# Kernel tuning notes

Hardware: AMD Instinct MI355X
Metric: run time of the kernel (lower is better)

Reference implementation:

```python
import jax, jax.numpy as jnp
import numpy as np
import math

EPS = 1e-5

def _ln(x):
    # LayerNorm over last dim, no affine (elementwise_affine=False)
    m = jnp.mean(x, axis=-1, keepdims=True)
    v = jnp.var(x, axis=-1, keepdims=True)
    return (x - m) / jnp.sqrt(v + EPS)

def setup_inputs() -> dict:
    key = jax.random.key(0)
    ks = jax.random.split(key, 12)
    bs, P, L, D, H, V = 32, 256, 32, 128, 128, 300
    std = 1.0 / math.sqrt(H)
    xav = math.sqrt(2.0 / ((V + 1) + D))
    emb = jax.random.normal(ks[2], (V + 1, D), jnp.float32) * xav
    emb = emb.at[V].set(0.0)  # padding_idx row
    u = lambda k, shp: jax.random.uniform(k, shp, jnp.float32, -std, std)
    return {
        "paths": jax.random.randint(ks[0], (bs, P, L), 0, V + 1),
        "paths_mask": jax.random.randint(ks[1], (bs, P), 1, L + 1),
        "emb": emb,
        "Wi": u(ks[3], (2 * H, D)), "bi": u(ks[4], (2 * H,)),
        "Wh": u(ks[5], (2 * H, H)), "bh": u(ks[6], (2 * H,)),
        "Ww": u(ks[7], (H, D)), "bw": u(ks[8], (H,)),
        "Wu": u(ks[9], (H, H)), "bu": u(ks[10], (H,)),
        "gamma": jnp.ones((2 * H,), jnp.float32),
        "beta": jnp.zeros((2 * H,), jnp.float32),
    }

def reference(paths, paths_mask, emb, Wi, bi, Wh, bh, Ww, bw, Wu, bu, gamma, beta):
    bs, P, L = paths.shape
    D = emb.shape[1]
    H = Ww.shape[0]
    B = bs * P
    # Embed and flatten paths: [L, B, D] (time-major for scan)
    x = emb[paths].reshape(B * L and (B, L, D))  # [B, L, D]
    x = jnp.transpose(x, (1, 0, 2))              # [L, B, D]
    # Input-dependent parts precomputed across all timesteps
    xi = _ln(jnp.einsum('lbd,gd->lbg', x, Wi) + bi)  # [L, B, 2H]
    xw = _ln(jnp.einsum('lbd,hd->lbh', x, Ww) + bw)  # [L, B, H]

    def step(h, xs_t):
        i2h_t, xw_t = xs_t
        h2h = _ln(h @ Wh.T + bh)
        gates = jax.nn.sigmoid(i2h_t + h2h)
        z = gates[:, :H]
        r = gates[:, H:]
        hu = _ln(h @ Wu.T + bu)
        h_hat = jnp.tanh(xw_t + r * hu)
        h_new = (1.0 - z) * h + z * h_hat
        return h_new, h_new

    h0 = jnp.zeros((B, H), x.dtype)
    _, ys = jax.lax.scan(step, h0, (xi, xw))      # ys: [L, B, H]
    lengths = paths_mask.reshape(-1)              # [B]
    out = ys[lengths - 1, jnp.arange(B)]          # [B, H] hidden at last valid step
    out = out.reshape(bs, P, H)
    # interleave forward/backward halves (relation-path pairing)
    fwd = jnp.concatenate([out[:, 0::2, :], out[:, 1::2, :]], axis=-1)
    bwd = jnp.concatenate([out[:, 1::2, :], out[:, 0::2, :]], axis=-1)
    res = jnp.zeros((bs, P, 2 * H), out.dtype)
    res = res.at[:, 0::2, :].set(fwd).at[:, 1::2, :].set(bwd)
    # final affine LayerNorm (gru_ln)
    m = jnp.mean(res, axis=-1, keepdims=True)
    v = jnp.var(res, axis=-1, keepdims=True)
    return (res - m) / jnp.sqrt(v + EPS) * gamma + beta
```

## Files before the change

### kernel.cpp

```cpp
#include <hip/hip_runtime.h>

typedef float  f32x4 __attribute__((ext_vector_type(4)));
typedef short  s16x8 __attribute__((ext_vector_type(8)));

__device__ __forceinline__ unsigned short bfb(float x) {
  unsigned u = __builtin_bit_cast(unsigned, x);
  return (unsigned short)((u + 0x7FFFu + ((u >> 16) & 1u)) >> 16);
}
__device__ __forceinline__ float fast_sig(float x) {
  float e = __builtin_amdgcn_exp2f(x * -1.44269504f);
  return __builtin_amdgcn_rcpf(1.f + e);
}
__device__ __forceinline__ float fast_tanh(float x) {
  float e = __builtin_amdgcn_exp2f(x * 2.88539008f);
  return 1.f - 2.f * __builtin_amdgcn_rcpf(1.f + e);
}

__global__ __launch_bounds__(1024) void sort_kernel(
    const int* __restrict__ pmask, int* __restrict__ perm)
{
  __shared__ int hist[33];
  __shared__ int base[33];
  const int tid = threadIdx.x;
  if (tid < 33) hist[tid] = 0;
  __syncthreads();
  for (int i = tid; i < 8192; i += 1024) atomicAdd(&hist[pmask[i]], 1);
  __syncthreads();
  if (tid == 0) {
    int acc = 0;
    for (int l = 1; l <= 32; ++l) { base[l] = acc; acc += hist[l]; }
  }
  __syncthreads();
  for (int i = tid; i < 8192; i += 1024) {
    const int pos = atomicAdd(&base[pmask[i]], 1);
    perm[pos] = i;
  }
}

__global__ __launch_bounds__(256) void tab_kernel(
    const float* __restrict__ emb,
    const float* __restrict__ Wi, const float* __restrict__ bi,
    const float* __restrict__ Ww, const float* __restrict__ bw,
    const float* __restrict__ Wh, const float* __restrict__ Wu,
    float* __restrict__ xi_tab, float* __restrict__ xw_tab,
    s16x8* __restrict__ frags)
{
  if (blockIdx.x >= 301) {
    const int T = blockIdx.x - 301;
    const int lane = threadIdx.x;
    if (lane >= 64) return;
    const int a = lane & 15, s = lane >> 4;
    const float* rowp[3];
    rowp[0] = Wh + (16 * T + a) * 128;
    rowp[1] = Wh + (128 + 16 * T + a) * 128;
    rowp[2] = Wu + (16 * T + a) * 128;
    #pragma unroll
    for (int mat = 0; mat < 3; ++mat) {
      #pragma unroll
      for (int kk = 0; kk < 4; ++kk) {
        const float* src = rowp[mat] + 32 * kk + 8 * s;
        const float4 A = *(const float4*)src;
        const float4 B = *(const float4*)(src + 4);
        s16x8 v;
        v[0] = (short)bfb(A.x); v[1] = (short)bfb(A.y);
        v[2] = (short)bfb(A.z); v[3] = (short)bfb(A.w);
        v[4] = (short)bfb(B.x); v[5] = (short)bfb(B.y);
        v[6] = (short)bfb(B.z); v[7] = (short)bfb(B.w);
        frags[((mat * 8 + T) * 4 + kk) * 64 + lane] = v;
      }
    }
    return;
  }

  const int v = blockIdx.x;
  const int g = threadIdx.x;
  const float4* er = (const float4*)(emb + v * 128);

  float acc = bi[g];
  const float4* wr = (const float4*)(Wi + g * 128);
  #pragma unroll 8
  for (int j = 0; j < 32; ++j) {
    float4 e = er[j], w4 = wr[j];
    acc = fmaf(e.x, w4.x, acc); acc = fmaf(e.y, w4.y, acc);
    acc = fmaf(e.z, w4.z, acc); acc = fmaf(e.w, w4.w, acc);
  }
  float accw = 0.f;
  if (g < 128) {
    accw = bw[g];
    const float4* wr2 = (const float4*)(Ww + g * 128);
    #pragma unroll 8
    for (int j = 0; j < 32; ++j) {
      float4 e = er[j], w4 = wr2[j];
      accw = fmaf(e.x, w4.x, accw); accw = fmaf(e.y, w4.y, accw);
      accw = fmaf(e.z, w4.z, accw); accw = fmaf(e.w, w4.w, accw);
    }
  }
  __shared__ float rs[4][2], rw[2][2];
  float s = acc, q = acc * acc;
  #pragma unroll
  for (int m = 1; m < 64; m <<= 1) { s += __shfl_xor(s, m); q += __shfl_xor(q, m); }
  if ((threadIdx.x & 63) == 0) { rs[threadIdx.x >> 6][0] = s; rs[threadIdx.x >> 6][1] = q; }
  float sw_ = accw, qw_ = accw * accw;
  #pragma unroll
  for (int m = 1; m < 64; m <<= 1) { sw_ += __shfl_xor(sw_, m); qw_ += __shfl_xor(qw_, m); }
  if (g < 128 && (g & 63) == 0) { rw[g >> 6][0] = sw_; rw[g >> 6][1] = qw_; }
  __syncthreads();
  const float SH = rs[0][0] + rs[1][0] + rs[2][0] + rs[3][0];
  const float QH = rs[0][1] + rs[1][1] + rs[2][1] + rs[3][1];
  const float mH = SH * (1.f / 256.f);
  const float rH = rsqrtf(fmaxf(QH * (1.f / 256.f) - mH * mH, 0.f) + 1e-5f);
  xi_tab[v * 256 + g] = (acc - mH) * rH;
  if (g < 128) {
    const float SW = rw[0][0] + rw[1][0], QW = rw[0][1] + rw[1][1];
    const float mW = SW * (1.f / 128.f);
    const float rW = rsqrtf(fmaxf(QW * (1.f / 128.f) - mW * mW, 0.f) + 1e-5f);
    xw_tab[v * 128 + g] = (accw - mW) * rW;
  }
}

__global__ __launch_bounds__(256, 2) void rec_kernel(
    const int* __restrict__ paths, const int* __restrict__ pmask,
    const int* __restrict__ perm,
    const float* __restrict__ bh, const float* __restrict__ bu,
    const float* __restrict__ xi_tab, const float* __restrict__ xw_tab,
    const s16x8* __restrict__ frags,
    float* __restrict__ out)
{
  __shared__ unsigned char hbuf[4096];
  __shared__ alignas(16) float red[4][16][4];
  __shared__ int plT[512];

  const int tid  = threadIdx.x;
  const int w    = tid >> 6;
  const int lane = tid & 63;
  const int s    = lane >> 4;
  const int r    = lane & 15;
  const int grp  = (blockIdx.x < 256) ? blockIdx.x : 767 - blockIdx.x;
  const int base = grp * 16;
  const int gb0  = 32 * w + 4 * s;

  s16x8 wz[2][4], wr2[2][4], wu2[2][4];
  #pragma unroll
  for (int u = 0; u < 2; ++u) {
    const int T = 2 * w + u;
    #pragma unroll
    for (int kk = 0; kk < 4; ++kk) {
      wz[u][kk]  = frags[((0 * 8 + T) * 4 + kk) * 64 + lane];
      wr2[u][kk] = frags[((1 * 8 + T) * 4 + kk) * 64 + lane];
      wu2[u][kk] = frags[((2 * 8 + T) * 4 + kk) * 64 + lane];
    }
  }

  for (int k = tid; k < 512; k += 256)
    plT[(k >> 4) * 16 + (k & 15)] = paths[perm[base + (k & 15)] * 32 + (k >> 4)];
  ((uint4*)hbuf)[tid] = uint4{0u, 0u, 0u, 0u};

  const int ri  = perm[base + r];
  const int len = pmask[ri];
  const int len_max = __shfl(len, 15);

  f32x4 bz[2], br2[2], bu2[2];
  #pragma unroll
  for (int u = 0; u < 2; ++u) {
    bz[u]  = *(const f32x4*)(bh + gb0 + 16 * u);
    br2[u] = *(const f32x4*)(bh + 128 + gb0 + 16 * u);
    bu2[u] = *(const f32x4*)(bu + gb0 + 16 * u);
  }

  int hoff[4];
  #pragma unroll
  for (int kk = 0; kk < 4; ++kk)
    hoff[kk] = r * 256 + (((4 * kk + s) ^ r) << 4);
  int hwadr[2];
  #pragma unroll
  for (int u = 0; u < 2; ++u)
    hwadr[u] = r * 256 + (((4 * w + 2 * u + (s >> 1)) ^ r) << 4) + (s & 1) * 8;

  float hreg[2][4] = {{0.f, 0.f, 0.f, 0.f}, {0.f, 0.f, 0.f, 0.f}};
  float* orow = out + (size_t)ri * 256 + gb0;

  __syncthreads();

  f32x4 xiz[2], xir[2], xwv[2];
  {
    const int p = plT[r];
    #pragma unroll
    for (int u = 0; u < 2; ++u) {
      xiz[u] = *(const f32x4*)(xi_tab + p * 256 + gb0 + 16 * u);
      xir[u] = *(const f32x4*)(xi_tab + p * 256 + 128 + gb0 + 16 * u);
      xwv[u] = *(const f32x4*)(xw_tab + p * 128 + gb0 + 16 * u);
    }
  }

  #pragma unroll 1
  for (int t = 0; t < len_max; ++t) {
    f32x4 az[2] = {}, ar[2] = {}, au[2] = {};
    #pragma unroll
    for (int kk = 0; kk < 4; ++kk) {
      const s16x8 hb = *(const s16x8*)(hbuf + hoff[kk]);
      #pragma unroll
      for (int u = 0; u < 2; ++u) {
        az[u] = __builtin_amdgcn_mfma_f32_16x16x32_bf16(wz[u][kk],  hb, az[u], 0, 0, 0);
        ar[u] = __builtin_amdgcn_mfma_f32_16x16x32_bf16(wr2[u][kk], hb, ar[u], 0, 0, 0);
        au[u] = __builtin_amdgcn_mfma_f32_16x16x32_bf16(wu2[u][kk], hb, au[u], 0, 0, 0);
      }
    }

    float sH = 0.f, qH = 0.f, sU = 0.f, qU = 0.f;
    #pragma unroll
    for (int u = 0; u < 2; ++u) {
      #pragma unroll
      for (int i = 0; i < 4; ++i) {
        az[u][i] += bz[u][i];  sH += az[u][i]; qH = fmaf(az[u][i], az[u][i], qH);
        ar[u][i] += br2[u][i]; sH += ar[u][i]; qH = fmaf(ar[u][i], ar[u][i], qH);
        au[u][i] += bu2[u][i]; sU += au[u][i]; qU = fmaf(au[u][i], au[u][i], qU);
      }
    }
    sH += __shfl_xor(sH, 16); qH += __shfl_xor(qH, 16);
    sU += __shfl_xor(sU, 16); qU += __shfl_xor(qU, 16);
    sH += __shfl_xor(sH, 32); qH += __shfl_xor(qH, 32);
    sU += __shfl_xor(sU, 32); qU += __shfl_xor(qU, 32);
    if (lane < 16) *(f32x4*)&red[w][r][0] = f32x4{sH, qH, sU, qU};

    const int tn = (t + 1 < len_max) ? t + 1 : t;
    const int pn = plT[tn * 16 + r];
    f32x4 nxiz[2], nxir[2], nxwv[2];
    #pragma unroll
    for (int u = 0; u < 2; ++u) {
      nxiz[u] = *(const f32x4*)(xi_tab + pn * 256 + gb0 + 16 * u);
      nxir[u] = *(const f32x4*)(xi_tab + pn * 256 + 128 + gb0 + 16 * u);
      nxwv[u] = *(const f32x4*)(xw_tab + pn * 128 + gb0 + 16 * u);
    }

    __syncthreads();

    float SH = 0.f, QH = 0.f, SU = 0.f, QU = 0.f;
    #pragma unroll
    for (int ww = 0; ww < 4; ++ww) {
      const f32x4 rr4 = *(const f32x4*)&red[ww][r][0];
      SH += rr4[0]; QH += rr4[1]; SU += rr4[2]; QU += rr4[3];
    }
    const float mH = SH * (1.f / 256.f);
    const float rsH = rsqrtf(fmaxf(QH * (1.f / 256.f) - mH * mH, 0.f) + 1e-5f);
    const float cH = -mH * rsH;
    const float mU = SU * (1.f / 128.f);
    const float rsU = rsqrtf(fmaxf(QU * (1.f / 128.f) - mU * mU, 0.f) + 1e-5f);
    const float cU = -mU * rsU;

    float hn[2][4];
    #pragma unroll
    for (int u = 0; u < 2; ++u) {
      #pragma unroll
      for (int i = 0; i < 4; ++i) {
        const float zg = fast_sig(xiz[u][i] + fmaf(az[u][i], rsH, cH));
        const float rg = fast_sig(xir[u][i] + fmaf(ar[u][i], rsH, cH));
        const float hu = fmaf(au[u][i], rsU, cU);
        const float hh = fast_tanh(fmaf(rg, hu, xwv[u][i]));
        hn[u][i] = fmaf(zg, hh - hreg[u][i], hreg[u][i]);
      }
    }
    if (t == len - 1) {
      #pragma unroll
      for (int u = 0; u < 2; ++u)
        *(float4*)(orow + 16 * u) = float4{hn[u][0], hn[u][1], hn[u][2], hn[u][3]};
    }

    #pragma unroll
    for (int u = 0; u < 2; ++u) {
      const unsigned lo  = (unsigned)bfb(hn[u][0]) | ((unsigned)bfb(hn[u][1]) << 16);
      const unsigned hi2 = (unsigned)bfb(hn[u][2]) | ((unsigned)bfb(hn[u][3]) << 16);
      *(uint2*)(hbuf + hwadr[u]) = uint2{lo, hi2};
      #pragma unroll
      for (int i = 0; i < 4; ++i) hreg[u][i] = hn[u][i];
      xiz[u] = nxiz[u]; xir[u] = nxir[u]; xwv[u] = nxwv[u];
    }
    __syncthreads();
  }
}

__global__ __launch_bounds__(256) void out_kernel(
    const float* __restrict__ gamma, const float* __restrict__ beta,
    float* __restrict__ out)
{
  const int tid = threadIdx.x;
  const int lane = tid & 63;
  const int m = blockIdx.x * 4 + (tid >> 6);
  float* pa = out + (size_t)(2 * m) * 256;
  float* pb = pa + 256;
  const float oa0 = pa[lane], oa1 = pa[64 + lane];
  const float ob0 = pb[lane], ob1 = pb[64 + lane];
  float s = oa0 + oa1 + ob0 + ob1;
  float q = oa0 * oa0 + oa1 * oa1 + ob0 * ob0 + ob1 * ob1;
  #pragma unroll
  for (int msk = 1; msk < 64; msk <<= 1) { s += __shfl_xor(s, msk); q += __shfl_xor(q, msk); }
  const float mean = s * (1.f / 256.f);
  const float rstd = rsqrtf(fmaxf(q * (1.f / 256.f) - mean * mean, 0.f) + 1e-5f);
  const float g0 = gamma[lane], g1 = gamma[64 + lane], g2 = gamma[128 + lane], g3 = gamma[192 + lane];
  const float b0 = beta[lane],  b1 = beta[64 + lane],  b2 = beta[128 + lane],  b3 = beta[192 + lane];
  const float na0 = (oa0 - mean) * rstd, na1 = (oa1 - mean) * rstd;
  const float nb0 = (ob0 - mean) * rstd, nb1 = (ob1 - mean) * rstd;
  pa[lane]       = na0 * g0 + b0;
  pa[64 + lane]  = na1 * g1 + b1;
  pa[128 + lane] = nb0 * g2 + b2;
  pa[192 + lane] = nb1 * g3 + b3;
  pb[lane]       = nb0 * g0 + b0;
  pb[64 + lane]  = nb1 * g1 + b1;
  pb[128 + lane] = na0 * g2 + b2;
  pb[192 + lane] = na1 * g3 + b3;
}

extern "C" void kernel_launch(void* const* d_in, const int* in_sizes, int n_in,
                              void* d_out, int out_size, void* d_ws, size_t ws_size,
                              hipStream_t stream) {
  const int*   paths = (const int*)d_in[0];
  const int*   pmask = (const int*)d_in[1];
  const float* emb   = (const float*)d_in[2];
  const float* Wi    = (const float*)d_in[3];
  const float* bi    = (const float*)d_in[4];
  const float* Wh    = (const float*)d_in[5];
  const float* bh    = (const float*)d_in[6];
  const float* Ww    = (const float*)d_in[7];
  const float* bw    = (const float*)d_in[8];
  const float* Wu    = (const float*)d_in[9];
  const float* bu    = (const float*)d_in[10];
  const float* gamma = (const float*)d_in[11];
  const float* beta  = (const float*)d_in[12];
  float* out = (float*)d_out;

  float* xi_tab = (float*)d_ws;
  float* xw_tab = xi_tab + 301 * 256;
  s16x8* frags  = (s16x8*)((char*)d_ws + 462336);
  int*   perm   = (int*)((char*)d_ws + 560640);

  hipLaunchKernelGGL(sort_kernel, dim3(1), dim3(1024), 0, stream, pmask, perm);
  hipLaunchKernelGGL(tab_kernel, dim3(309), dim3(256), 0, stream,
                     emb, Wi, bi, Ww, bw, Wh, Wu, xi_tab, xw_tab, frags);
  hipLaunchKernelGGL(rec_kernel, dim3(512), dim3(256), 0, stream,
                     paths, pmask, perm, bh, bu, xi_tab, xw_tab, frags, out);
  hipLaunchKernelGGL(out_kernel, dim3(1024), dim3(256), 0, stream, gamma, beta, out);
}
```

Before: 76.70 us.

## Fold sort into table kernel, replace shuffle reduction with LDS partials, hoist prefetch

After: 75.17 us. -2.0%, faster.

```diff
diff --git a/kernel.cpp b/kernel.cpp
--- a/kernel.cpp
+++ b/kernel.cpp
@@ -14,27 +14,6 @@
 __device__ __forceinline__ float fast_tanh(float x) {
   float e = __builtin_amdgcn_exp2f(x * 2.88539008f);
   return 1.f - 2.f * __builtin_amdgcn_rcpf(1.f + e);
-}
-
-__global__ __launch_bounds__(1024) void sort_kernel(
-    const int* __restrict__ pmask, int* __restrict__ perm)
-{
-  __shared__ int hist[33];
-  __shared__ int base[33];
-  const int tid = threadIdx.x;
-  if (tid < 33) hist[tid] = 0;
-  __syncthreads();
-  for (int i = tid; i < 8192; i += 1024) atomicAdd(&hist[pmask[i]], 1);
-  __syncthreads();
-  if (tid == 0) {
-    int acc = 0;
-    for (int l = 1; l <= 32; ++l) { base[l] = acc; acc += hist[l]; }
-  }
-  __syncthreads();
-  for (int i = tid; i < 8192; i += 1024) {
-    const int pos = atomicAdd(&base[pmask[i]], 1);
-    perm[pos] = i;
-  }
 }
 
 __global__ __launch_bounds__(256) void tab_kernel(
@@ -42,9 +21,29 @@
     const float* __restrict__ Wi, const float* __restrict__ bi,
     const float* __restrict__ Ww, const float* __restrict__ bw,
     const float* __restrict__ Wh, const float* __restrict__ Wu,
+    const int* __restrict__ pmask, int* __restrict__ perm,
     float* __restrict__ xi_tab, float* __restrict__ xw_tab,
     s16x8* __restrict__ frags)
 {
+  if (blockIdx.x == 309) {
+    __shared__ int hist[33];
+    __shared__ int base2[33];
+    const int tid = threadIdx.x;
+    if (tid < 33) hist[tid] = 0;
+    __syncthreads();
+    for (int i = tid; i < 8192; i += 256) atomicAdd(&hist[pmask[i]], 1);
+    __syncthreads();
+    if (tid == 0) {
+      int acc = 0;
+      for (int l = 1; l <= 32; ++l) { base2[l] = acc; acc += hist[l]; }
+    }
+    __syncthreads();
+    for (int i = tid; i < 8192; i += 256) {
+      const int pos = atomicAdd(&base2[pmask[i]], 1);
+      perm[pos] = i;
+    }
+    return;
+  }
   if (blockIdx.x >= 301) {
     const int T = blockIdx.x - 301;
     const int lane = threadIdx.x;
@@ -127,7 +126,7 @@
     float* __restrict__ out)
 {
   __shared__ unsigned char hbuf[4096];
-  __shared__ alignas(16) float red[4][16][4];
+  __shared__ alignas(16) float red[4][4][16][4];
   __shared__ int plT[512];
 
   const int tid  = threadIdx.x;
@@ -194,6 +193,16 @@
 
   #pragma unroll 1
   for (int t = 0; t < len_max; ++t) {
+    const int tn = (t + 1 < len_max) ? t + 1 : t;
+    const int pn = plT[tn * 16 + r];
+    f32x4 nxiz[2], nxir[2], nxwv[2];
+    #pragma unroll
+    for (int u = 0; u < 2; ++u) {
+      nxiz[u] = *(const f32x4*)(xi_tab + pn * 256 + gb0 + 16 * u);
+      nxir[u] = *(const f32x4*)(xi_tab + pn * 256 + 128 + gb0 + 16 * u);
+      nxwv[u] = *(const f32x4*)(xw_tab + pn * 128 + gb0 + 16 * u);
+    }
+
     f32x4 az[2] = {}, ar[2] = {}, au[2] = {};
     #pragma unroll
     for (int kk = 0; kk < 4; ++kk) {
@@ -216,35 +225,23 @@
         au[u][i] += bu2[u][i]; sU += au[u][i]; qU = fmaf(au[u][i], au[u][i], qU);
       }
     }
-    sH += __shfl_xor(sH, 16); qH += __shfl_xor(qH, 16);
-    sU += __shfl_xor(sU, 16); qU += __shfl_xor(qU, 16);
-    sH += __shfl_xor(sH, 32); qH += __shfl_xor(qH, 32);
-    sU += __shfl_xor(sU, 32); qU += __shfl_xor(qU, 32);
-    if (lane < 16) *(f32x4*)&red[w][r][0] = f32x4{sH, qH, sU, qU};
-
-    const int tn = (t + 1 < len_max) ? t + 1 : t;
-    const int pn = plT[tn * 16 + r];
-    f32x4 nxiz[2], nxir[2], nxwv[2];
-    #pragma unroll
-    for (int u = 0; u < 2; ++u) {
-      nxiz[u] = *(const f32x4*)(xi_tab + pn * 256 + gb0 + 16 * u);
-      nxir[u] = *(const f32x4*)(xi_tab + pn * 256 + 128 + gb0 + 16 * u);
-      nxwv[u] = *(const f32x4*)(xw_tab + pn * 128 + gb0 + 16 * u);
-    }
-
-    __syncthreads();
-
-    float SH = 0.f, QH = 0.f, SU = 0.f, QU = 0.f;
-    #pragma unroll
-    for (int ww = 0; ww < 4; ++ww) {
-      const f32x4 rr4 = *(const f32x4*)&red[ww][r][0];
-      SH += rr4[0]; QH += rr4[1]; SU += rr4[2]; QU += rr4[3];
-    }
-    const float mH = SH * (1.f / 256.f);
-    const float rsH = rsqrtf(fmaxf(QH * (1.f / 256.f) - mH * mH, 0.f) + 1e-5f);
+    *(f32x4*)&red[w][s][r][0] = f32x4{sH, qH, sU, qU};
+
+    __syncthreads();
+
+    f32x4 acc0 = *(const f32x4*)&red[0][0][r][0];
+    f32x4 acc1 = *(const f32x4*)&red[0][1][r][0];
+    #pragma unroll
+    for (int c = 2; c < 16; c += 2) {
+      acc0 += *(const f32x4*)&red[c >> 2][c & 3][r][0];
+      acc1 += *(const f32x4*)&red[(c + 1) >> 2][(c + 1) & 3][r][0];
+    }
+    const f32x4 S = acc0 + acc1;
+    const float mH = S[0] * (1.f / 256.f);
+    const float rsH = rsqrtf(fmaxf(S[1] * (1.f / 256.f) - mH * mH, 0.f) + 1e-5f);
     const float cH = -mH * rsH;
-    const float mU = SU * (1.f / 128.f);
-    const float rsU = rsqrtf(fmaxf(QU * (1.f / 128.f) - mU * mU, 0.f) + 1e-5f);
+    const float mU = S[2] * (1.f / 128.f);
+    const float rsU = rsqrtf(fmaxf(S[3] * (1.f / 128.f) - mU * mU, 0.f) + 1e-5f);
     const float cU = -mU * rsU;
 
     float hn[2][4];
@@ -332,9 +329,8 @@
   s16x8* frags  = (s16x8*)((char*)d_ws + 462336);
   int*   perm   = (int*)((char*)d_ws + 560640);
 
-  hipLaunchKernelGGL(sort_kernel, dim3(1), dim3(1024), 0, stream, pmask, perm);
-  hipLaunchKernelGGL(tab_kernel, dim3(309), dim3(256), 0, stream,
-                     emb, Wi, bi, Ww, bw, Wh, Wu, xi_tab, xw_tab, frags);
+  hipLaunchKernelGGL(tab_kernel, dim3(310), dim3(256), 0, stream,
+                     emb, Wi, bi, Ww, bw, Wh, Wu, pmask, perm, xi_tab, xw_tab, frags);
   hipLaunchKernelGGL(rec_kernel, dim3(512), dim3(256), 0, stream,
                      paths, pmask, perm, bh, bu, xi_tab, xw_tab, frags, out);
   hipLaunchKernelGGL(out_kernel, dim3(1024), dim3(256), 0, stream, gamma, beta, out);
```
